# Kernel optimization log

Hardware: AMD Instinct MI355X
Metric: run time of the kernel (lower is better)

Reference implementation:

```python
import jax, jax.numpy as jnp
import numpy as np

B, S, D, H = 2, 2048, 1024, 16
DH = D // H  # per-head depth = 64


def setup_inputs() -> dict:
    key = jax.random.key(0)
    ks = jax.random.split(key, 10)
    s = 1.0 / np.sqrt(D)
    return {
        "q_in": jax.random.normal(ks[0], (B, S, D), jnp.float32),
        "k_in": jax.random.normal(ks[1], (B, S, D), jnp.float32),
        "v_in": jax.random.normal(ks[2], (B, S, D), jnp.float32),
        "mask": jnp.zeros((B, 1, S, S), jnp.float32),
        "Wq": jax.random.normal(ks[3], (D, D), jnp.float32) * s,
        "bq": jnp.zeros((D,), jnp.float32),
        "Wk": jax.random.normal(ks[4], (D, D), jnp.float32) * s,
        "bk": jnp.zeros((D,), jnp.float32),
        "Wv": jax.random.normal(ks[5], (D, D), jnp.float32) * s,
        "bv": jnp.zeros((D,), jnp.float32),
        "Wo": jax.random.normal(ks[6], (D, D), jnp.float32) * s,
        "bo": jnp.zeros((D,), jnp.float32),
    }


def _split_heads(x):
    # [B,S,D] -> [B,H,S,DH]
    b, s, _ = x.shape
    return x.reshape(b, s, H, DH).transpose(0, 2, 1, 3)


def reference(q_in, k_in, v_in, mask, Wq, bq, Wk, bk, Wv, bv, Wo, bo):
    q = _split_heads(q_in @ Wq + bq)
    k = _split_heads(k_in @ Wk + bk)
    v = _split_heads(v_in @ Wv + bv)
    logits = jnp.einsum("bhqd,bhkd->bhqk", q, k) / jnp.sqrt(jnp.float32(DH))
    logits = logits + mask * -1e9
    attn = jax.nn.softmax(logits, axis=-1)
    ctx = jnp.einsum("bhqk,bhkd->bhqd", attn, v)  # [B,H,S,DH]
    concat = ctx.transpose(0, 2, 1, 3).reshape(q_in.shape[0], -1, D)
    out = concat @ Wo + bo  # dropout is identity at inference
    return out, attn
```

## Files before the change

kernel.cpp:

```cpp
#include <hip/hip_runtime.h>
#include <hip/hip_bf16.h>

static constexpr int cB = 2, cS = 2048, cD = 1024, cH = 16, cDH = 64;

typedef __attribute__((ext_vector_type(4))) float f32x4;
typedef __attribute__((ext_vector_type(8))) short s16x8;
typedef unsigned long long u64;
typedef unsigned short u16;

__device__ inline f32x4 mfma16(s16x8 a, s16x8 b, f32x4 c) {
  return __builtin_amdgcn_mfma_f32_16x16x32_bf16(a, b, c, 0, 0, 0);
}

__device__ inline u16 f2bf(float x) {
  unsigned u = __float_as_uint(x);
  u += 0x7FFFu + ((u >> 16) & 1u);
  return (u16)(u >> 16);
}

__device__ inline f32x4 zero4() { f32x4 z; z[0] = z[1] = z[2] = z[3] = 0.f; return z; }

__device__ inline void gload16(const void* src, void* dst) {
  __builtin_amdgcn_global_load_lds((const __attribute__((address_space(1))) void*)src,
                                   (__attribute__((address_space(3))) void*)dst, 16, 0, 0);
}

#define LDT 72


__global__ __launch_bounds__(256) void wt_kernel(const float* __restrict__ W,
                                                 u16* __restrict__ Wt) {
  __shared__ float tile[32][33];
  int tx = threadIdx.x, ty = threadIdx.y;
  int r0 = blockIdx.y * 32, c0 = blockIdx.x * 32;
  for (int i = ty; i < 32; i += 8)
    tile[i][tx] = W[(size_t)(r0 + i) * cD + c0 + tx];
  __syncthreads();
  for (int i = ty; i < 32; i += 8)
    Wt[(size_t)(c0 + i) * cD + r0 + tx] = f2bf(tile[tx][i]);
}

__global__ __launch_bounds__(256) void maskflag_kernel(const float* __restrict__ mask,
                                                       unsigned char* __restrict__ flags) {
  int blk = blockIdx.x;
  int b = blk >> 10, qt = (blk >> 5) & 31, kt = blk & 31;
  int t = threadIdx.x;
  int r = t >> 2, c0 = (t & 3) * 16;
  const float4* p = (const float4*)(mask + ((size_t)b * cS + qt * 64 + r) * cS + kt * 64 + c0);
  int any = 0;
  for (int j = 0; j < 4; ++j) {
    float4 v = p[j];
    any |= (v.x != 0.f) | (v.y != 0.f) | (v.z != 0.f) | (v.w != 0.f);
  }
  __shared__ int sred;
  if (t == 0) sred = 0;
  __syncthreads();
  if (any) atomicOr(&sred, 1);
  __syncthreads();
  if (t == 0) flags[blk] = (unsigned char)sred;
}

template<bool AFP32, bool OUTF32>
__global__ __launch_bounds__(256) void gemm128(const void* __restrict__ Ap,
                                               const u16* __restrict__ Bt,
                                               const float* __restrict__ bias,
                                               void* __restrict__ outp,
                                               float scale, int vt_mode) {
  __shared__ __attribute__((aligned(16))) u16 As[128 * 64];
  __shared__ __attribute__((aligned(16))) u16 Bs[128 * 64];
  int t = threadIdx.x;
  int w = t >> 6, l = t & 63, g = l >> 4, li = l & 15;
  int bm = blockIdx.x & 31, bn = blockIdx.x >> 5;
  int m0 = bm * 128, n0 = bn * 128;
  int wr = w >> 1, wc = w & 1;

  f32x4 acc[4][4];
  for (int i = 0; i < 4; ++i)
    for (int j = 0; j < 4; ++j) acc[i][j] = zero4();

  for (int kk = 0; kk < cD; kk += 64) {
    if (AFP32) {
      const float* X = (const float*)Ap;
      int ar = t >> 1, ak0 = (t & 1) * 32;
      const float* asrc = X + (size_t)(m0 + ar) * cD + kk + ak0;
      int sw = ar & 7;
      for (int j = 0; j < 4; ++j) {
        float4 x0 = ((const float4*)asrc)[2 * j];
        float4 x1 = ((const float4*)asrc)[2 * j + 1];
        union { s16x8 v; u16 h[8]; } s;
        s.h[0] = f2bf(x0.x); s.h[1] = f2bf(x0.y); s.h[2] = f2bf(x0.z); s.h[3] = f2bf(x0.w);
        s.h[4] = f2bf(x1.x); s.h[5] = f2bf(x1.y); s.h[6] = f2bf(x1.z); s.h[7] = f2bf(x1.w);
        int chunk = (ak0 >> 3) + j;
        *(s16x8*)&As[ar * 64 + ((chunk ^ sw) * 8)] = s.v;
      }
    } else {
      const u16* X = (const u16*)Ap;
      for (int is = 0; is < 4; ++is) {
        int row = w * 32 + is * 8 + (l >> 3);
        int chunk = l & 7;
        const u16* src = X + (size_t)(m0 + row) * cD + kk + ((chunk ^ (row & 7)) * 8);
        gload16(src, &As[(w * 32 + is * 8) * 64]);
      }
    }
    for (int is = 0; is < 4; ++is) {
      int row = w * 32 + is * 8 + (l >> 3);
      int chunk = l & 7;
      const u16* src = Bt + (size_t)(n0 + row) * cD + kk + ((chunk ^ (row & 7)) * 8);
      gload16(src, &Bs[(w * 32 + is * 8) * 64]);
    }
    __syncthreads();
    for (int c = 0; c < 2; ++c) {
      s16x8 af[4], bf[4];
      for (int mi = 0; mi < 4; ++mi) {
        int r = wr * 64 + mi * 16 + li;
        af[mi] = *(const s16x8*)&As[r * 64 + (((c * 4 + g) ^ (r & 7)) * 8)];
      }
      for (int ni = 0; ni < 4; ++ni) {
        int r = wc * 64 + ni * 16 + li;
        bf[ni] = *(const s16x8*)&Bs[r * 64 + (((c * 4 + g) ^ (r & 7)) * 8)];
      }
      for (int mi = 0; mi < 4; ++mi)
        for (int ni = 0; ni < 4; ++ni)
          acc[mi][ni] = mfma16(af[mi], bf[ni], acc[mi][ni]);
    }
    __syncthreads();
  }

  for (int ni = 0; ni < 4; ++ni) {
    int n = n0 + wc * 64 + ni * 16 + li;
    float bv = bias[n];
    for (int mi = 0; mi < 4; ++mi) {
      for (int r = 0; r < 4; ++r) {
        int m = m0 + wr * 64 + mi * 16 + g * 4 + r;
        float val = acc[mi][ni][r] + bv;
        if (OUTF32) {
          ((float*)outp)[(size_t)m * cD + n] = val;
        } else {
          val *= scale;
          int b = m >> 11, s = m & 2047;
          int h = n >> 6, d = n & 63;
          size_t idx = vt_mode ? ((size_t)(b * cH + h) * cDH + d) * cS + s
                               : ((size_t)(b * cH + h) * cS + s) * cDH + d;
          ((u16*)outp)[idx] = f2bf(val);
        }
      }
    }
  }
}

__global__ __launch_bounds__(256) void attn_kernel(const u16* __restrict__ Q,
                                                   const u16* __restrict__ K,
                                                   const u16* __restrict__ Vt,
                                                   const float* __restrict__ mask,
                                                   const unsigned char* __restrict__ flags,
                                                   float* __restrict__ attn,
                                                   u16* __restrict__ ctx) {
  __shared__ __attribute__((aligned(16))) u16 Kl[64 * 64];
  __shared__ __attribute__((aligned(16))) u16 Vl[64 * 64];
  __shared__ __attribute__((aligned(16))) u16 Pl[4][16][LDT];
  int t = threadIdx.x;
  int w = t >> 6, l = t & 63, g = l >> 4, li = l & 15;
  int blk = blockIdx.x;
  int bh = blk >> 5, qt = blk & 31;
  int b = bh >> 4;
  int qbase = qt * 64;
  const u16* Qh = Q + (size_t)bh * cS * cDH;
  const u16* Kh = K + (size_t)bh * cS * cDH;
  const u16* Vh = Vt + (size_t)bh * cDH * cS;
  const unsigned char* fl = flags + (b << 10) + qt * 32;

  s16x8 qf[2];
  {
    const u16* qp = Qh + (size_t)(qbase + w * 16 + li) * cDH;
    qf[0] = *(const s16x8*)(qp + 8 * g);
    qf[1] = *(const s16x8*)(qp + 32 + 8 * g);
  }
  int srow8 = l >> 3, schunk = l & 7;

  float rs[4] = {0.f, 0.f, 0.f, 0.f};
  for (int kt = 0; kt < 32; ++kt) {
    for (int is = 0; is < 2; ++is) {
      int row = w * 16 + is * 8 + srow8;
      const u16* src = Kh + (size_t)(kt * 64 + row) * cDH + ((schunk ^ (row & 7)) * 8);
      gload16(src, &Kl[(w * 16 + is * 8) * 64]);
    }
    __syncthreads();
    f32x4 acc[4];
    for (int nt = 0; nt < 4; ++nt) acc[nt] = zero4();
    for (int c = 0; c < 2; ++c)
      for (int nt = 0; nt < 4; ++nt) {
        int r = nt * 16 + li;
        s16x8 bfr = *(const s16x8*)&Kl[r * 64 + (((c * 4 + g) ^ (r & 7)) * 8)];
        acc[nt] = mfma16(qf[c], bfr, acc[nt]);
      }
    bool um = fl[kt] != 0;
    for (int nt = 0; nt < 4; ++nt)
      for (int r = 0; r < 4; ++r) {
        float lv = acc[nt][r];
        if (um) {
          int qg = qbase + w * 16 + g * 4 + r;
          int kg = kt * 64 + nt * 16 + li;
          lv += mask[((size_t)b * cS + qg) * cS + kg] * -1e9f;
        }
        rs[r] += __expf(lv);
      }
    __syncthreads();
  }
  for (int r = 0; r < 4; ++r) {
    for (int msk = 1; msk < 16; msk <<= 1) rs[r] += __shfl_xor(rs[r], msk, 64);
    rs[r] = 1.f / rs[r];
  }

  f32x4 cacc[4];
  for (int dt = 0; dt < 4; ++dt) cacc[dt] = zero4();
  float* attn_base = attn + (size_t)bh * cS * cS;
  for (int kt = 0; kt < 32; ++kt) {
    for (int is = 0; is < 2; ++is) {
      int row = w * 16 + is * 8 + srow8;
      const u16* ksrc = Kh + (size_t)(kt * 64 + row) * cDH + ((schunk ^ (row & 7)) * 8);
      gload16(ksrc, &Kl[(w * 16 + is * 8) * 64]);
      const u16* vsrc = Vh + (size_t)row * cS + kt * 64 + ((schunk ^ (row & 7)) * 8);
      gload16(vsrc, &Vl[(w * 16 + is * 8) * 64]);
    }
    __syncthreads();
    f32x4 acc[4];
    for (int nt = 0; nt < 4; ++nt) acc[nt] = zero4();
    for (int c = 0; c < 2; ++c)
      for (int nt = 0; nt < 4; ++nt) {
        int r = nt * 16 + li;
        s16x8 bfr = *(const s16x8*)&Kl[r * 64 + (((c * 4 + g) ^ (r & 7)) * 8)];
        acc[nt] = mfma16(qf[c], bfr, acc[nt]);
      }
    bool um = fl[kt] != 0;
    for (int nt = 0; nt < 4; ++nt) {
      int kg = kt * 64 + nt * 16 + li;
      for (int r = 0; r < 4; ++r) {
        float lv = acc[nt][r];
        int qg = qbase + w * 16 + g * 4 + r;
        if (um) lv += mask[((size_t)b * cS + qg) * cS + kg] * -1e9f;
        float p = __expf(lv) * rs[r];
        attn_base[(size_t)qg * cS + kg] = p;
        Pl[w][g * 4 + r][nt * 16 + li] = f2bf(p);
      }
    }
    for (int c = 0; c < 2; ++c) {
      s16x8 pa = *(const s16x8*)&Pl[w][li][c * 32 + 8 * g];
      for (int dt = 0; dt < 4; ++dt) {
        int r = dt * 16 + li;
        s16x8 bv2 = *(const s16x8*)&Vl[r * 64 + (((c * 4 + g) ^ (r & 7)) * 8)];
        cacc[dt] = mfma16(pa, bv2, cacc[dt]);
      }
    }
    __syncthreads();
  }

  int h = bh & 15;
  for (int dt = 0; dt < 4; ++dt)
    for (int r = 0; r < 4; ++r) {
      int s = qbase + w * 16 + g * 4 + r;
      int d = dt * 16 + li;
      ctx[((size_t)(b * cS + s)) * cD + h * 64 + d] = f2bf(cacc[dt][r]);
    }
}

extern "C" void kernel_launch(void* const* d_in, const int* in_sizes, int n_in,
                              void* d_out, int out_size, void* d_ws, size_t ws_size,
                              hipStream_t stream) {
  const float* q_in = (const float*)d_in[0];
  const float* k_in = (const float*)d_in[1];
  const float* v_in = (const float*)d_in[2];
  const float* mask = (const float*)d_in[3];
  const float* Wq = (const float*)d_in[4];
  const float* bq = (const float*)d_in[5];
  const float* Wk = (const float*)d_in[6];
  const float* bk = (const float*)d_in[7];
  const float* Wv = (const float*)d_in[8];
  const float* bv = (const float*)d_in[9];
  const float* Wo = (const float*)d_in[10];
  const float* bo = (const float*)d_in[11];

  float* out = (float*)d_out;
  float* attn = out + (size_t)cB * cS * cD;

  const size_t MATB = (size_t)cB * cS * cD * 2;
  const size_t WB = (size_t)cD * cD * 2;
  char* ws = (char*)d_ws;
  u16* WqT = (u16*)(ws);
  u16* WkT = (u16*)(ws + WB);
  u16* WvT = (u16*)(ws + 2 * WB);
  u16* WoT = (u16*)(ws + 3 * WB);
  u16* wsQ  = (u16*)(ws + 4 * WB);
  u16* wsK  = (u16*)(ws + 4 * WB + MATB);
  u16* wsVt = (u16*)(ws + 4 * WB + 2 * MATB);
  u16* wsC  = (u16*)(ws + 4 * WB + 3 * MATB);
  unsigned char* flags = (unsigned char*)(ws + 4 * WB + 4 * MATB);
  const size_t REQUIRED = 4 * WB + 4 * MATB + 2048;
  if (ws_size < REQUIRED) return;

  dim3 tb(32, 8);
  wt_kernel<<<dim3(32, 32), tb, 0, stream>>>(Wq, WqT);
  wt_kernel<<<dim3(32, 32), tb, 0, stream>>>(Wk, WkT);
  wt_kernel<<<dim3(32, 32), tb, 0, stream>>>(Wv, WvT);
  wt_kernel<<<dim3(32, 32), tb, 0, stream>>>(Wo, WoT);
  maskflag_kernel<<<2048, 256, 0, stream>>>(mask, flags);

  gemm128<true, false><<<256, 256, 0, stream>>>(q_in, WqT, bq, wsQ, 0.125f, 0);
  gemm128<true, false><<<256, 256, 0, stream>>>(k_in, WkT, bk, wsK, 1.0f, 0);
  gemm128<true, false><<<256, 256, 0, stream>>>(v_in, WvT, bv, wsVt, 1.0f, 1);

  attn_kernel<<<1024, 256, 0, stream>>>(wsQ, wsK, wsVt, mask, flags, attn, wsC);

  gemm128<false, true><<<256, 256, 0, stream>>>(wsC, WoT, bo, out, 1.0f, 0);
}
```

Measured before the change: 404.9 us.

## Double-buffer K/V tiles and compute transposed S so P stays in registers

After: 427.5 us. 1.06x slower.

```diff
diff --git a/kernel.cpp b/kernel.cpp
--- a/kernel.cpp
+++ b/kernel.cpp
@@ -24,8 +24,6 @@
   __builtin_amdgcn_global_load_lds((const __attribute__((address_space(1))) void*)src,
                                    (__attribute__((address_space(3))) void*)dst, 16, 0, 0);
 }
-
-#define LDT 72
 
 
 __global__ __launch_bounds__(256) void wt_kernel(const float* __restrict__ W,
@@ -148,16 +146,15 @@
   }
 }
 
-__global__ __launch_bounds__(256) void attn_kernel(const u16* __restrict__ Q,
-                                                   const u16* __restrict__ K,
-                                                   const u16* __restrict__ Vt,
-                                                   const float* __restrict__ mask,
-                                                   const unsigned char* __restrict__ flags,
-                                                   float* __restrict__ attn,
-                                                   u16* __restrict__ ctx) {
-  __shared__ __attribute__((aligned(16))) u16 Kl[64 * 64];
-  __shared__ __attribute__((aligned(16))) u16 Vl[64 * 64];
-  __shared__ __attribute__((aligned(16))) u16 Pl[4][16][LDT];
+__global__ __launch_bounds__(256, 3) void attn_kernel(const u16* __restrict__ Q,
+                                                      const u16* __restrict__ K,
+                                                      const u16* __restrict__ Vt,
+                                                      const float* __restrict__ mask,
+                                                      const unsigned char* __restrict__ flags,
+                                                      float* __restrict__ attn,
+                                                      u16* __restrict__ ctx) {
+  __shared__ __attribute__((aligned(16))) u16 Kl[2][64 * 64];
+  __shared__ __attribute__((aligned(16))) u16 Vl[2][64 * 64];
   int t = threadIdx.x;
   int w = t >> 6, l = t & 63, g = l >> 4, li = l & 15;
   int blk = blockIdx.x;
@@ -176,82 +173,105 @@
     qf[1] = *(const s16x8*)(qp + 32 + 8 * g);
   }
   int srow8 = l >> 3, schunk = l & 7;
-
-  float rs[4] = {0.f, 0.f, 0.f, 0.f};
+  int q_lane = qbase + w * 16 + li;
+
+  float racc = 0.f;
+  for (int is = 0; is < 2; ++is) {
+    int row = w * 16 + is * 8 + srow8;
+    gload16(Kh + (size_t)row * cDH + ((schunk ^ (row & 7)) * 8), &Kl[0][(w * 16 + is * 8) * 64]);
+  }
+  __syncthreads();
+  int cur = 0;
   for (int kt = 0; kt < 32; ++kt) {
-    for (int is = 0; is < 2; ++is) {
-      int row = w * 16 + is * 8 + srow8;
-      const u16* src = Kh + (size_t)(kt * 64 + row) * cDH + ((schunk ^ (row & 7)) * 8);
-      gload16(src, &Kl[(w * 16 + is * 8) * 64]);
-    }
+    if (kt + 1 < 32) {
+      for (int is = 0; is < 2; ++is) {
+        int row = w * 16 + is * 8 + srow8;
+        gload16(Kh + (size_t)((kt + 1) * 64 + row) * cDH + ((schunk ^ (row & 7)) * 8),
+                &Kl[cur ^ 1][(w * 16 + is * 8) * 64]);
+      }
+    }
+    f32x4 acc[4];
+    for (int mt = 0; mt < 4; ++mt) acc[mt] = zero4();
+    for (int c = 0; c < 2; ++c)
+      for (int mt = 0; mt < 4; ++mt) {
+        int r = mt * 16 + li;
+        s16x8 kf = *(const s16x8*)&Kl[cur][r * 64 + (((c * 4 + g) ^ (r & 7)) * 8)];
+        acc[mt] = mfma16(kf, qf[c], acc[mt]);
+      }
+    bool um = fl[kt] != 0;
+    for (int mt = 0; mt < 4; ++mt)
+      for (int r = 0; r < 4; ++r) {
+        float lv = acc[mt][r];
+        if (um) lv += mask[((size_t)b * cS + q_lane) * cS + kt * 64 + mt * 16 + 4 * g + r] * -1e9f;
+        racc += __expf(lv);
+      }
     __syncthreads();
-    f32x4 acc[4];
-    for (int nt = 0; nt < 4; ++nt) acc[nt] = zero4();
-    for (int c = 0; c < 2; ++c)
-      for (int nt = 0; nt < 4; ++nt) {
-        int r = nt * 16 + li;
-        s16x8 bfr = *(const s16x8*)&Kl[r * 64 + (((c * 4 + g) ^ (r & 7)) * 8)];
-        acc[nt] = mfma16(qf[c], bfr, acc[nt]);
-      }
-    bool um = fl[kt] != 0;
-    for (int nt = 0; nt < 4; ++nt)
-      for (int r = 0; r < 4; ++r) {
-        float lv = acc[nt][r];
-        if (um) {
-          int qg = qbase + w * 16 + g * 4 + r;
-          int kg = kt * 64 + nt * 16 + li;
-          lv += mask[((size_t)b * cS + qg) * cS + kg] * -1e9f;
-        }
-        rs[r] += __expf(lv);
-      }
-    __syncthreads();
-  }
-  for (int r = 0; r < 4; ++r) {
-    for (int msk = 1; msk < 16; msk <<= 1) rs[r] += __shfl_xor(rs[r], msk, 64);
-    rs[r] = 1.f / rs[r];
-  }
+    cur ^= 1;
+  }
+  racc += __shfl_xor(racc, 16, 64);
+  racc += __shfl_xor(racc, 32, 64);
+  float rs = 1.f / racc;
 
   f32x4 cacc[4];
   for (int dt = 0; dt < 4; ++dt) cacc[dt] = zero4();
-  float* attn_base = attn + (size_t)bh * cS * cS;
+  float* attn_row = attn + (size_t)bh * cS * cS + (size_t)q_lane * cS;
+  for (int is = 0; is < 2; ++is) {
+    int row = w * 16 + is * 8 + srow8;
+    gload16(Kh + (size_t)row * cDH + ((schunk ^ (row & 7)) * 8), &Kl[0][(w * 16 + is * 8) * 64]);
+    gload16(Vh + (size_t)row * cS + ((schunk ^ (row & 7)) * 8), &Vl[0][(w * 16 + is * 8) * 64]);
+  }
+  __syncthreads();
+  cur = 0;
   for (int kt = 0; kt < 32; ++kt) {
-    for (int is = 0; is < 2; ++is) {
-      int row = w * 16 + is * 8 + srow8;
-      const u16* ksrc = Kh + (size_t)(kt * 64 + row) * cDH + ((schunk ^ (row & 7)) * 8);
-      gload16(ksrc, &Kl[(w * 16 + is * 8) * 64]);
-      const u16* vsrc = Vh + (size_t)row * cS + kt * 64 + ((schunk ^ (row & 7)) * 8);
-      gload16(vsrc, &Vl[(w * 16 + is * 8) * 64]);
+    if (kt + 1 < 32) {
+      for (int is = 0; is < 2; ++is) {
+        int row = w * 16 + is * 8 + srow8;
+        gload16(Kh + (size_t)((kt + 1) * 64 + row) * cDH + ((schunk ^ (row & 7)) * 8),
+                &Kl[cur ^ 1][(w * 16 + is * 8) * 64]);
+        gload16(Vh + (size_t)row * cS + (kt + 1) * 64 + ((schunk ^ (row & 7)) * 8),
+                &Vl[cur ^ 1][(w * 16 + is * 8) * 64]);
+      }
+    }
+    f32x4 acc[4];
+    for (int mt = 0; mt < 4; ++mt) acc[mt] = zero4();
+    for (int c = 0; c < 2; ++c)
+      for (int mt = 0; mt < 4; ++mt) {
+        int r = mt * 16 + li;
+        s16x8 kf = *(const s16x8*)&Kl[cur][r * 64 + (((c * 4 + g) ^ (r & 7)) * 8)];
+        acc[mt] = mfma16(kf, qf[c], acc[mt]);
+      }
+    bool um = fl[kt] != 0;
+    s16x8 pa[2];
+    for (int c = 0; c < 2; ++c) {
+      union { s16x8 v; u16 h[8]; } pk;
+      for (int hh = 0; hh < 2; ++hh) {
+        int mt = c * 2 + hh;
+        f32x4 pv;
+        for (int r = 0; r < 4; ++r) {
+          float lv = acc[mt][r];
+          if (um) lv += mask[((size_t)b * cS + q_lane) * cS + kt * 64 + mt * 16 + 4 * g + r] * -1e9f;
+          float p = __expf(lv) * rs;
+          pv[r] = p;
+          pk.h[hh * 4 + r] = f2bf(p);
+        }
+        *(f32x4*)(attn_row + kt * 64 + mt * 16 + 4 * g) = pv;
+      }
+      pa[c] = pk.v;
+    }
+    for (int c = 0; c < 2; ++c) {
+      for (int dt = 0; dt < 4; ++dt) {
+        int row = dt * 16 + li;
+        const u16* rb = &Vl[cur][row * 64];
+        int o0 = (((c * 4 + 0 + (g >> 1)) ^ (li & 7)) * 8) + (g & 1) * 4;
+        int o1 = (((c * 4 + 2 + (g >> 1)) ^ (li & 7)) * 8) + (g & 1) * 4;
+        union { s16x8 v; u64 qq[2]; } vf;
+        vf.qq[0] = *(const u64*)(rb + o0);
+        vf.qq[1] = *(const u64*)(rb + o1);
+        cacc[dt] = mfma16(pa[c], vf.v, cacc[dt]);
+      }
     }
     __syncthreads();
-    f32x4 acc[4];
-    for (int nt = 0; nt < 4; ++nt) acc[nt] = zero4();
-    for (int c = 0; c < 2; ++c)
-      for (int nt = 0; nt < 4; ++nt) {
-        int r = nt * 16 + li;
-        s16x8 bfr = *(const s16x8*)&Kl[r * 64 + (((c * 4 + g) ^ (r & 7)) * 8)];
-        acc[nt] = mfma16(qf[c], bfr, acc[nt]);
-      }
-    bool um = fl[kt] != 0;
-    for (int nt = 0; nt < 4; ++nt) {
-      int kg = kt * 64 + nt * 16 + li;
-      for (int r = 0; r < 4; ++r) {
-        float lv = acc[nt][r];
-        int qg = qbase + w * 16 + g * 4 + r;
-        if (um) lv += mask[((size_t)b * cS + qg) * cS + kg] * -1e9f;
-        float p = __expf(lv) * rs[r];
-        attn_base[(size_t)qg * cS + kg] = p;
-        Pl[w][g * 4 + r][nt * 16 + li] = f2bf(p);
-      }
-    }
-    for (int c = 0; c < 2; ++c) {
-      s16x8 pa = *(const s16x8*)&Pl[w][li][c * 32 + 8 * g];
-      for (int dt = 0; dt < 4; ++dt) {
-        int r = dt * 16 + li;
-        s16x8 bv2 = *(const s16x8*)&Vl[r * 64 + (((c * 4 + g) ^ (r & 7)) * 8)];
-        cacc[dt] = mfma16(pa, bv2, cacc[dt]);
-      }
-    }
-    __syncthreads();
+    cur ^= 1;
   }
 
   int h = bh & 15;
@@ -301,6 +321,7 @@
   wt_kernel<<<dim3(32, 32), tb, 0, stream>>>(Wq, WqT);
   wt_kernel<<<dim3(32, 32), tb, 0, stream>>>(Wk, WkT);
   wt_kernel<<<dim3(32, 32), tb, 0, stream>>>(Wv, WvT);
+  wt_kernel<<<dim3(32, 32), tb, 0, stream>>>(Wv, WvT);
   wt_kernel<<<dim3(32, 32), tb, 0, stream>>>(Wo, WoT);
   maskflag_kernel<<<2048, 256, 0, stream>>>(mask, flags);
 
```
